# Performance work log

Hardware: AMD Instinct MI355X
Metric: run time of the kernel (lower is better)

## Reference

```python
import jax, jax.numpy as jnp
import numpy as np

N_NODES = 20000   # atoms
N_EDGES = 300000  # directed edges within cutoff
N_TRIP = 500000   # triplets (k->j->i)
H = 128           # hidden_channels
NR = 6            # num_radial
NS = 7            # num_spherical
NB = 8            # num_bilinear
OUT = 128         # out_channels
NLAY = 3          # num_layers in OutputBlock
NOB = 2           # num_blocks + 1 output blocks


def _silu(v):
    return v * jax.nn.sigmoid(v)  # swish


def setup_inputs() -> dict:
    key = jax.random.key(0)
    ks = jax.random.split(key, 20)
    s = lambda fan: np.float32(1.0 / np.sqrt(fan))
    inp = {}
    inp["x"] = jax.random.normal(ks[0], (N_EDGES, H), jnp.float32)
    inp["rbf"] = jax.random.uniform(ks[1], (N_EDGES, NR), jnp.float32)
    inp["sbf"] = jax.random.uniform(ks[2], (N_TRIP, NS * NR), jnp.float32)
    inp["i"] = jax.random.randint(ks[3], (N_EDGES,), 0, N_NODES)
    inp["idx_kj"] = jax.random.randint(ks[4], (N_TRIP,), 0, N_EDGES)
    inp["idx_ji"] = jax.random.randint(ks[5], (N_TRIP,), 0, N_EDGES)
    # Interaction params (weights stored [in, out] so y = x @ W)
    inp["W_rbf"] = jax.random.normal(ks[6], (NR, H), jnp.float32) * s(NR)
    inp["W_sbf"] = jax.random.normal(ks[7], (NS * NR, NB), jnp.float32) * s(NS * NR)
    inp["W_kj"] = jax.random.normal(ks[8], (H, H), jnp.float32) * s(H)
    inp["b_kj"] = jnp.zeros((H,), jnp.float32)
    inp["W_ji"] = jax.random.normal(ks[9], (H, H), jnp.float32) * s(H)
    inp["b_ji"] = jnp.zeros((H,), jnp.float32)
    inp["W_bil"] = jax.random.normal(ks[10], (H, NB, H), jnp.float32) * np.float32(2.0 / H)
    inp["W_lin"] = jax.random.normal(ks[11], (H, H), jnp.float32) * s(H)
    inp["b_lin"] = jnp.zeros((H,), jnp.float32)
    # OutputBlock params, stacked over the NOB blocks
    inp["out_lin_rbf"] = jax.random.normal(ks[12], (NOB, NR, H), jnp.float32) * s(NR)
    inp["out_lins_W"] = jax.random.normal(ks[13], (NOB, NLAY, H, H), jnp.float32) * s(H)
    inp["out_lins_b"] = jnp.zeros((NOB, NLAY, H), jnp.float32)
    inp["out_lin"] = jax.random.normal(ks[14], (NOB, H, OUT), jnp.float32) * s(H)
    return inp


def _output_block(xe, rbf, i, lin_rbf, lins_W, lins_b, lin_out):
    # OutputBlock.forward: gate edge features by rbf projection, scatter to nodes
    g = (rbf @ lin_rbf) * xe              # [E, H]
    g = jax.ops.segment_sum(g, i, num_segments=N_NODES)  # [N, H]
    for li in range(NLAY):
        g = _silu(g @ lins_W[li] + lins_b[li])
    return g @ lin_out                    # [N, OUT]


def _interaction(x, rbf, sbf, idx_kj, idx_ji,
                 W_rbf, W_sbf, W_kj, b_kj, W_ji, b_ji, W_bil, W_lin, b_lin):
    r = rbf @ W_rbf                       # [E, H]
    sproj = sbf @ W_sbf                   # [T, NB]
    x_ji = _silu(x @ W_ji + b_ji)         # [E, H]
    x_kj = _silu(x @ W_kj + b_kj) * r     # [E, H]
    xg = x_kj[idx_kj]                     # [T, H] triplet gather
    # einsum('wj,wl,ijl->wi', sproj, xg, W_bil) without the [T, H, NB] blowup:
    # loop over the small fixed bilinear dim NB, accumulating [T, H]
    t = jnp.zeros((xg.shape[0], H), xg.dtype)
    for jb in range(NB):
        t = t + sproj[:, jb:jb + 1] * (xg @ W_bil[:, jb, :].T)
    agg = jax.ops.segment_sum(t, idx_ji, num_segments=N_EDGES)  # scatter to edges
    return _silu((x_ji + agg) @ W_lin + b_lin)


def reference(x, rbf, sbf, i, idx_kj, idx_ji,
              W_rbf, W_sbf, W_kj, b_kj, W_ji, b_ji, W_bil, W_lin, b_lin,
              out_lin_rbf, out_lins_W, out_lins_b, out_lin):
    P = _output_block(x, rbf, i, out_lin_rbf[0], out_lins_W[0], out_lins_b[0], out_lin[0])
    x2 = _interaction(x, rbf, sbf, idx_kj, idx_ji,
                      W_rbf, W_sbf, W_kj, b_kj, W_ji, b_ji, W_bil, W_lin, b_lin)
    P = P + _output_block(x2, rbf, i, out_lin_rbf[1], out_lins_W[1], out_lins_b[1], out_lin[1])
    return P.sum(axis=0)  # batch=None path: global readout [OUT]
```

## Files before the change

### kernel.cpp

```cpp
#include <hip/hip_runtime.h>
#include <hip/hip_fp16.h>

#define NN 20000
#define NE 300000
#define NT 500000
#define HD 128
#define NRR 6
#define NSNRD 42
#define NBB 8

using f16x8 = __attribute__((ext_vector_type(8))) _Float16;
using f32x4 = __attribute__((ext_vector_type(4))) float;

__device__ __forceinline__ float silu_f(float v){ return v / (1.f + __expf(-v)); }

__device__ __forceinline__ void pk_add(__half2* p, float lo, float hi){
  __half2 h = __floats2half2_rn(lo, hi);
  unsigned int b = *reinterpret_cast<unsigned int*>(&h);
  asm volatile("global_atomic_pk_add_f16 %0, %1, off" :: "v"(p), "v"(b) : "memory");
}

__device__ __forceinline__ void gload16(const void* g, char* lds_dst){
  __builtin_amdgcn_global_load_lds(
    (const __attribute__((address_space(1))) void*)g,
    (__attribute__((address_space(3))) void*)lds_dst, 16, 0, 0);
}

__global__ void k_x16(const float* __restrict__ x, __half* __restrict__ xh){
  long i = ((long)blockIdx.x*256 + threadIdx.x)*8;
  if(i < (long)NE*HD){
    float4 a = *(const float4*)(x+i), b = *(const float4*)(x+i+4);
    __half h8[8];
    h8[0]=__float2half(a.x); h8[1]=__float2half(a.y);
    h8[2]=__float2half(a.z); h8[3]=__float2half(a.w);
    h8[4]=__float2half(b.x); h8[5]=__float2half(b.y);
    h8[6]=__float2half(b.z); h8[7]=__float2half(b.w);
    *(float4*)(xh+i) = *(float4*)h8;
  }
}

__global__ void k_wb2(const float* __restrict__ Wb, __half* __restrict__ WB2){
  int idx = blockIdx.x*256 + threadIdx.x;
  int l = idx & 127, i = (idx>>7) & 127, jb = idx>>14;
  WB2[jb*16384 + i*128 + l] = __float2half(Wb[i*1024 + jb*128 + l]);
}

__global__ void k_wT(const float* __restrict__ Wkj, const float* __restrict__ Wji,
                     const float* __restrict__ Wlin, __half* __restrict__ WkjT,
                     __half* __restrict__ WjiT, __half* __restrict__ WlinT){
  int idx = blockIdx.x*256 + threadIdx.x;
  int which = idx>>14, rem = idx & 16383;
  int i = rem>>7, k = rem & 127;
  const float* src = which==0 ? Wkj : (which==1 ? Wji : Wlin);
  __half* dst = which==0 ? WkjT : (which==1 ? WjiT : WlinT);
  dst[rem] = __float2half(src[k*HD + i]);
}

__global__ void k_wT6(const float* __restrict__ olW, __half* __restrict__ dst){
  int idx = blockIdx.x*256 + threadIdx.x;
  int lw = idx>>14, rem = idx & 16383;
  int i = rem>>7, k = rem & 127;
  dst[lw*16384 + rem] = __float2half(olW[lw*16384 + k*HD + i]);
}

#define EROWS 128
#define PRE_A 0
#define PRE_B 32768
#define PRE_RBF 65536
#define PRE_WR 68608
#define PRE_LS 71680
#define PRE_NID 74752
#define SH_PRE 75264
__global__ __launch_bounds__(512,4)
void k_edge_pre(const __half* __restrict__ xh, const float* __restrict__ rbf,
                const int* __restrict__ nid, const __half* __restrict__ WkjT,
                const float* __restrict__ bkj, const float* __restrict__ Wrbf,
                const float* __restrict__ lrbf0, __half* __restrict__ xkj,
                __half* __restrict__ g0){
  extern __shared__ char sm[];
  int tid = threadIdx.x;
  long e0 = (long)blockIdx.x * EROWS;
  for(int c=tid;c<2048;c+=512){
    int i=c>>4, cc=c&15;
    float4 v = *(const float4*)(WkjT + i*128 + cc*8);
    *(float4*)(sm + PRE_B + ((i*256+cc*16)^((i&7)<<4))) = v;
  }
  for(int c=tid;c<2048;c+=512){
    int r=c>>4, cc=c&15; long e=e0+r;
    float4 v = (e<NE) ? *(const float4*)(xh + e*HD + cc*8)
                      : (float4){0.f,0.f,0.f,0.f};
    *(float4*)(sm + PRE_A + ((r*256+cc*16)^((r&7)<<4))) = v;
  }
  float* rbft=(float*)(sm+PRE_RBF);
  for(int q=tid;q<EROWS*NRR;q+=512){ long e=e0+q/NRR; rbft[q]=(e<NE)? rbf[e*NRR + q%NRR] : 0.f; }
  float* wrbf=(float*)(sm+PRE_WR);
  for(int q=tid;q<NRR*HD;q+=512) wrbf[q]=Wrbf[q];
  float* ls0=(float*)(sm+PRE_LS);
  for(int q=tid;q<NRR*HD;q+=512) ls0[q]=lrbf0[q];
  int* nids=(int*)(sm+PRE_NID);
  if (tid < EROWS){ long e=e0+tid; nids[tid]=(e<NE)? nid[e] : 0; }
  __syncthreads();
  int lane=tid&63, wid=tid>>6, wr=wid>>1, wc=wid&1;
  f16x8 af[2][4];
  #pragma unroll
  for(int rt=0;rt<2;rt++){
    int r = wr*32 + rt*16 + (lane&15);
    #pragma unroll
    for(int ks=0;ks<4;ks++)
      af[rt][ks] = *(const f16x8*)(sm + PRE_A + ((r*256 + (ks*4+(lane>>4))*16)^((r&7)<<4)));
  }
  f32x4 acc[2][4];
  #pragma unroll
  for(int rt=0;rt<2;rt++){
    #pragma unroll
    for(int ct=0;ct<4;ct++) acc[rt][ct]=(f32x4){0.f,0.f,0.f,0.f};
  }
  #pragma unroll
  for(int ct=0;ct<4;ct++){
    int i = wc*64 + ct*16 + (lane&15);
    #pragma unroll
    for(int ks=0;ks<4;ks++){
      f16x8 b = *(const f16x8*)(sm + PRE_B + ((i*256 + (ks*4+(lane>>4))*16)^((i&7)<<4)));
      acc[0][ct] = __builtin_amdgcn_mfma_f32_16x16x32_f16(af[0][ks], b, acc[0][ct], 0,0,0);
      acc[1][ct] = __builtin_amdgcn_mfma_f32_16x16x32_f16(af[1][ks], b, acc[1][ct], 0,0,0);
    }
  }
  #pragma unroll
  for(int rt=0;rt<2;rt++){
    #pragma unroll
    for(int j=0;j<4;j++){
      int rloc = wr*32 + rt*16 + (lane>>4)*4 + j;
      long e = e0 + rloc;
      bool ok = (e<NE);
      int nb = nids[rloc];
      #pragma unroll
      for(int ct=0;ct<4;ct++){
        int h = wc*64 + ct*16 + (lane&15);
        float v = silu_f(acc[rt][ct][j] + bkj[h]);
        float r2=0.f, gate=0.f;
        #pragma unroll
        for(int q=0;q<NRR;q++){
          float rb = rbft[rloc*NRR+q];
          r2   += rb*wrbf[q*HD+h];
          gate += rb*ls0[q*HD+h];
        }
        float xval = __half2float(*(const __half*)(sm + PRE_A +
                       ((rloc*256 + (h>>3)*16)^((rloc&7)<<4)) + (h&7)*2));
        float w1 = v*r2;
        float w2 = gate*xval;
        float p1 = __shfl_xor(w1, 1, 64);
        float p2 = __shfl_xor(w2, 1, 64);
        if(ok && !(lane&1)){
          *(__half2*)(xkj + e*HD + h) = __floats2half2_rn(w1, p1);
          pk_add((__half2*)(g0 + (long)nb*HD + h), w2, p2);
        }
      }
    }
  }
}

#define TROWS 128
#define OFF_BUF 0
#define OFF_SP 49152
#define OFF_KJ 53248
#define OFF_JI 53760
#define OFF_WSB 54272
#define SH_TRIP 55616
__global__ __launch_bounds__(512,4)
void k_triplet_mfma(const __half* __restrict__ xkj, const float* __restrict__ sbf,
                    const float* __restrict__ Wsbf,
                    const int* __restrict__ ikj, const int* __restrict__ iji,
                    const __half* __restrict__ WB2, __half* __restrict__ agg){
  extern __shared__ char sm[];
  int tid = threadIdx.x;
  long t0 = (long)blockIdx.x * TROWS;
  int* kjs = (int*)(sm + OFF_KJ);
  int* jis = (int*)(sm + OFF_JI);
  if (tid < TROWS){
    int ok = (t0 + tid) < NT;
    kjs[tid] = ok ? ikj[t0+tid] : 0;
    jis[tid] = ok ? iji[t0+tid] : -1;
  }
  float* sbuf = (float*)(sm + OFF_BUF);
  for(int q=tid;q<TROWS*NSNRD;q+=512){
    long t = t0 + q/NSNRD;
    sbuf[q] = (t<NT) ? sbf[t*NSNRD + q%NSNRD] : 0.f;
  }
  float* wsb = (float*)(sm + OFF_WSB);
  for(int q=tid;q<NSNRD*NBB;q+=512) wsb[q]=Wsbf[q];
  __syncthreads();
  float* spl = (float*)(sm + OFF_SP);
  {
    int r = tid>>2, j0 = (tid&3)*2;
    float a0=0.f,a1=0.f;
    for(int q=0;q<NSNRD;q++){
      float v = sbuf[r*NSNRD+q];
      a0 += v*wsb[q*NBB+j0];
      a1 += v*wsb[q*NBB+j0+1];
    }
    spl[r*NBB+j0]=a0; spl[r*NBB+j0+1]=a1;
  }
  __syncthreads();
  for(int c=tid;c<TROWS*16;c+=512){
    int w = c>>4, cc = c&15;
    float4 v = *(const float4*)(xkj + (long)kjs[w]*HD + cc*8);
    *(float4*)(sm + OFF_BUF + ((w*256 + cc*16)^((w&7)<<4))) = v;
  }
  __syncthreads();
  int lane = tid & 63;
  int wid = tid>>6, wr = wid>>1, wc = wid&1;
  f16x8 au[2][4];
  #pragma unroll
  for(int rt=0;rt<2;rt++){
    int w = wr*32 + rt*16 + (lane&15);
    #pragma unroll
    for(int ks=0;ks<4;ks++)
      au[rt][ks] = *(const f16x8*)(sm + OFF_BUF + ((w*256 + ks*64 + (lane>>4)*16)^((w&7)<<4)));
  }
  __syncthreads();
  #pragma unroll
  for(int u=0;u<2;u++){
    int c = u*512 + tid;
    int i = c>>3, lc = (c&7) ^ (i&7);
    gload16(WB2 + i*128 + lc*8,
            sm + OFF_BUF + u*8192 + (tid>>6)*1024);
  }
  #pragma unroll
  for(int u=0;u<2;u++){
    int c = u*512 + tid;
    int i = c>>3, lc = (c&7) ^ (i&7);
    gload16(WB2 + i*128 + 64 + lc*8,
            sm + OFF_BUF + 16384 + u*8192 + (tid>>6)*1024);
  }
  f32x4 acc[2][4];
  #pragma unroll
  for(int rt=0;rt<2;rt++){
    #pragma unroll
    for(int ct=0;ct<4;ct++) acc[rt][ct] = (f32x4){0.f,0.f,0.f,0.f};
  }
  float sr[2];
  #pragma unroll
  for(int p=0;p<16;p++){
    int jb = p>>1, h = p&1;
    if(h==0){
      #pragma unroll
      for(int rt=0;rt<2;rt++) sr[rt] = spl[(wr*32 + rt*16 + (lane&15))*NBB + jb];
    }
    if(p<15) asm volatile("s_waitcnt vmcnt(2)" ::: "memory");
    else     asm volatile("s_waitcnt vmcnt(0)" ::: "memory");
    __builtin_amdgcn_s_barrier();
    asm volatile("" ::: "memory");
    if(p+2 < 16){
      int np = p+2, njb = np>>1, nh = np&1;
      #pragma unroll
      for(int u=0;u<2;u++){
        int c = u*512 + tid;
        int i = c>>3, lc = (c&7) ^ (i&7);
        gload16(WB2 + njb*16384 + i*128 + nh*64 + lc*8,
                sm + OFF_BUF + ((p+2)%3)*16384 + u*8192 + (tid>>6)*1024);
      }
    }
    const char* bbase = sm + OFF_BUF + (p%3)*16384;
    #pragma unroll
    for(int ksl=0;ksl<2;ksl++){
      int ks = h*2 + ksl;
      f16x8 as2[2];
      #pragma unroll
      for(int rt=0;rt<2;rt++){
        _Float16 s = (_Float16)sr[rt];
        #pragma unroll
        for(int j=0;j<8;j++) as2[rt][j] = au[rt][ks][j]*s;
      }
      #pragma unroll
      for(int ct=0;ct<4;ct++){
        int it = wc*64 + ct*16 + (lane&15);
        int chunk = (ksl*4 + (lane>>4)) ^ (it&7);
        f16x8 b = *(const f16x8*)(bbase + it*128 + chunk*16);
        #pragma unroll
        for(int rt=0;rt<2;rt++)
          acc[rt][ct] = __builtin_amdgcn_mfma_f32_16x16x32_f16(as2[rt], b, acc[rt][ct], 0,0,0);
      }
    }
  }
  #pragma unroll
  for(int rt=0;rt<2;rt++){
    #pragma unroll
    for(int r=0;r<4;r++){
      int w = wr*32 + rt*16 + (lane>>4)*4 + r;
      int ji = jis[w];
      #pragma unroll
      for(int ct=0;ct<4;ct++){
        float v = acc[rt][ct][r];
        float p = __shfl_xor(v, 1, 64);
        if (ji >= 0 && !(lane&1))
          pk_add((__half2*)(agg + (long)ji*HD + wc*64 + ct*16 + (lane&15)), v, p);
      }
    }
  }
}

#define PO_A 0
#define PO_B 32768
#define PO_RBF 65536
#define PO_LS 68608
#define PO_NID 71680
#define SH_POST 72192
__global__ __launch_bounds__(512,4)
void k_edge_post(const __half* __restrict__ xh, const float* __restrict__ rbf,
                 const __half* __restrict__ aggh, const int* __restrict__ nid,
                 const __half* __restrict__ WjiT, const float* __restrict__ bji,
                 const __half* __restrict__ WlinT, const float* __restrict__ blin,
                 const float* __restrict__ lrbf1, __half* __restrict__ g1){
  extern __shared__ char sm[];
  int tid = threadIdx.x;
  long e0 = (long)blockIdx.x * EROWS;
  for(int c=tid;c<2048;c+=512){
    int i=c>>4, cc=c&15;
    float4 v = *(const float4*)(WjiT + i*128 + cc*8);
    *(float4*)(sm + PO_B + ((i*256+cc*16)^((i&7)<<4))) = v;
  }
  for(int c=tid;c<2048;c+=512){
    int r=c>>4, cc=c&15; long e=e0+r;
    float4 v = (e<NE) ? *(const float4*)(xh + e*HD + cc*8)
                      : (float4){0.f,0.f,0.f,0.f};
    *(float4*)(sm + PO_A + ((r*256+cc*16)^((r&7)<<4))) = v;
  }
  float* rbft=(float*)(sm+PO_RBF);
  for(int q=tid;q<EROWS*NRR;q+=512){ long e=e0+q/NRR; rbft[q]=(e<NE)? rbf[e*NRR + q%NRR] : 0.f; }
  float* ls1=(float*)(sm+PO_LS);
  for(int q=tid;q<NRR*HD;q+=512) ls1[q]=lrbf1[q];
  int* nids=(int*)(sm+PO_NID);
  if (tid < EROWS){ long e=e0+tid; nids[tid]=(e<NE)? nid[e] : 0; }
  __syncthreads();
  int lane=tid&63, wid=tid>>6, wr=wid>>1, wc=wid&1;
  f16x8 af[2][4];
  #pragma unroll
  for(int rt=0;rt<2;rt++){
    int r = wr*32 + rt*16 + (lane&15);
    #pragma unroll
    for(int ks=0;ks<4;ks++)
      af[rt][ks] = *(const f16x8*)(sm + PO_A + ((r*256 + (ks*4+(lane>>4))*16)^((r&7)<<4)));
  }
  f32x4 acc[2][4];
  #pragma unroll
  for(int rt=0;rt<2;rt++){
    #pragma unroll
    for(int ct=0;ct<4;ct++) acc[rt][ct]=(f32x4){0.f,0.f,0.f,0.f};
  }
  #pragma unroll
  for(int ct=0;ct<4;ct++){
    int i = wc*64 + ct*16 + (lane&15);
    #pragma unroll
    for(int ks=0;ks<4;ks++){
      f16x8 b = *(const f16x8*)(sm + PO_B + ((i*256 + (ks*4+(lane>>4))*16)^((i&7)<<4)));
      acc[0][ct] = __builtin_amdgcn_mfma_f32_16x16x32_f16(af[0][ks], b, acc[0][ct], 0,0,0);
      acc[1][ct] = __builtin_amdgcn_mfma_f32_16x16x32_f16(af[1][ks], b, acc[1][ct], 0,0,0);
    }
  }
  __syncthreads();
  #pragma unroll
  for(int rt=0;rt<2;rt++){
    #pragma unroll
    for(int j=0;j<4;j++){
      int rloc = wr*32 + rt*16 + (lane>>4)*4 + j;
      long e = e0 + rloc;
      #pragma unroll
      for(int ct=0;ct<4;ct++){
        int h = wc*64 + ct*16 + (lane&15);
        float v = silu_f(acc[rt][ct][j] + bji[h]);
        v += (e<NE) ? __half2float(aggh[e*HD + h]) : 0.f;
        int byo = ((rloc*256 + (h>>3)*16)^((rloc&7)<<4)) + (h&7)*2;
        *(__half*)(sm + PO_A + byo) = __float2half(v);
      }
    }
  }
  for(int c=tid;c<2048;c+=512){
    int i=c>>4, cc=c&15;
    float4 v = *(const float4*)(WlinT + i*128 + cc*8);
    *(float4*)(sm + PO_B + ((i*256+cc*16)^((i&7)<<4))) = v;
  }
  __syncthreads();
  f16x8 af2[2][4];
  #pragma unroll
  for(int rt=0;rt<2;rt++){
    int r = wr*32 + rt*16 + (lane&15);
    #pragma unroll
    for(int ks=0;ks<4;ks++)
      af2[rt][ks] = *(const f16x8*)(sm + PO_A + ((r*256 + (ks*4+(lane>>4))*16)^((r&7)<<4)));
  }
  f32x4 acc2[2][4];
  #pragma unroll
  for(int rt=0;rt<2;rt++){
    #pragma unroll
    for(int ct=0;ct<4;ct++) acc2[rt][ct]=(f32x4){0.f,0.f,0.f,0.f};
  }
  #pragma unroll
  for(int ct=0;ct<4;ct++){
    int i = wc*64 + ct*16 + (lane&15);
    #pragma unroll
    for(int ks=0;ks<4;ks++){
      f16x8 b = *(const f16x8*)(sm + PO_B + ((i*256 + (ks*4+(lane>>4))*16)^((i&7)<<4)));
      acc2[0][ct] = __builtin_amdgcn_mfma_f32_16x16x32_f16(af2[0][ks], b, acc2[0][ct], 0,0,0);
      acc2[1][ct] = __builtin_amdgcn_mfma_f32_16x16x32_f16(af2[1][ks], b, acc2[1][ct], 0,0,0);
    }
  }
  #pragma unroll
  for(int rt=0;rt<2;rt++){
    #pragma unroll
    for(int j=0;j<4;j++){
      int rloc = wr*32 + rt*16 + (lane>>4)*4 + j;
      long e = e0 + rloc;
      bool ok = (e<NE);
      int nb = nids[rloc];
      #pragma unroll
      for(int ct=0;ct<4;ct++){
        int h = wc*64 + ct*16 + (lane&15);
        float x2 = silu_f(acc2[rt][ct][j] + blin[h]);
        float gate = 0.f;
        #pragma unroll
        for(int q=0;q<NRR;q++) gate += rbft[rloc*NRR+q]*ls1[q*HD+h];
        float w = gate*x2;
        float p = __shfl_xor(w, 1, 64);
        if(ok && !(lane&1))
          pk_add((__half2*)(g1 + (long)nb*HD + h), w, p);
      }
    }
  }
}

#define SH_MLPM 65536
template<bool LAST>
__global__ __launch_bounds__(512,4)
void k_mlp_mfma(const __half* __restrict__ gin, const __half* __restrict__ WT,
                const float* __restrict__ b, __half* __restrict__ gout,
                float* __restrict__ s){
  extern __shared__ char sm[];
  int tid = threadIdx.x;
  long r0 = (long)blockIdx.x * EROWS;
  for(int c=tid;c<2048;c+=512){
    int i=c>>4, cc=c&15;
    float4 v = *(const float4*)(WT + i*128 + cc*8);
    *(float4*)(sm + 32768 + ((i*256+cc*16)^((i&7)<<4))) = v;
  }
  for(int c=tid;c<2048;c+=512){
    int r=c>>4, cc=c&15; long rr=r0+r;
    float4 v;
    if(rr<NN) v = *(const float4*)(gin + rr*HD + cc*8);
    else      v = (float4){0.f,0.f,0.f,0.f};
    *(float4*)(sm + ((r*256+cc*16)^((r&7)<<4))) = v;
  }
  __syncthreads();
  int lane=tid&63, wid=tid>>6, wr=wid>>1, wc=wid&1;
  f16x8 af[2][4];
  #pragma unroll
  for(int rt=0;rt<2;rt++){
    int r = wr*32 + rt*16 + (lane&15);
    #pragma unroll
    for(int ks=0;ks<4;ks++)
      af[rt][ks] = *(const f16x8*)(sm + ((r*256 + (ks*4+(lane>>4))*16)^((r&7)<<4)));
  }
  f32x4 acc[2][4];
  #pragma unroll
  for(int rt=0;rt<2;rt++){
    #pragma unroll
    for(int ct=0;ct<4;ct++) acc[rt][ct]=(f32x4){0.f,0.f,0.f,0.f};
  }
  #pragma unroll
  for(int ct=0;ct<4;ct++){
    int i = wc*64 + ct*16 + (lane&15);
    #pragma unroll
    for(int ks=0;ks<4;ks++){
      f16x8 bfr = *(const f16x8*)(sm + 32768 + ((i*256 + (ks*4+(lane>>4))*16)^((i&7)<<4)));
      acc[0][ct] = __builtin_amdgcn_mfma_f32_16x16x32_f16(af[0][ks], bfr, acc[0][ct], 0,0,0);
      acc[1][ct] = __builtin_amdgcn_mfma_f32_16x16x32_f16(af[1][ks], bfr, acc[1][ct], 0,0,0);
    }
  }
  if(LAST){
    float vsum[4];
    #pragma unroll
    for(int ct=0;ct<4;ct++) vsum[ct]=0.f;
    #pragma unroll
    for(int rt=0;rt<2;rt++){
      #pragma unroll
      for(int j=0;j<4;j++){
        int rloc = wr*32 + rt*16 + (lane>>4)*4 + j;
        long rr = r0 + rloc;
        #pragma unroll
        for(int ct=0;ct<4;ct++){
          int h = wc*64 + ct*16 + (lane&15);
          float v = (rr<NN) ? silu_f(acc[rt][ct][j] + b[h]) : 0.f;
          vsum[ct] += v;
        }
      }
    }
    #pragma unroll
    for(int ct=0;ct<4;ct++){
      vsum[ct] += __shfl_xor(vsum[ct], 16, 64);
      vsum[ct] += __shfl_xor(vsum[ct], 32, 64);
    }
    if((lane>>4)==0){
      #pragma unroll
      for(int ct=0;ct<4;ct++)
        atomicAdd(&s[wc*64 + ct*16 + (lane&15)], vsum[ct]);
    }
  } else {
    #pragma unroll
    for(int rt=0;rt<2;rt++){
      #pragma unroll
      for(int j=0;j<4;j++){
        int rloc = wr*32 + rt*16 + (lane>>4)*4 + j;
        long rr = r0 + rloc;
        bool ok = (rr<NN);
        #pragma unroll
        for(int ct=0;ct<4;ct++){
          int h = wc*64 + ct*16 + (lane&15);
          float v = silu_f(acc[rt][ct][j] + b[h]);
          float p = __shfl_xor(v, 1, 64);
          if(ok && !(lane&1))
            *(__half2*)(gout + rr*HD + h) = __floats2half2_rn(v, p);
        }
      }
    }
  }
}

__global__ void k_readout(const float* __restrict__ s0, const float* __restrict__ s1,
                          const float* __restrict__ OL, float* __restrict__ out){
  int o = threadIdx.x;
  float acc=0.f;
  for(int h=0;h<HD;h++) acc += s0[h]*OL[h*HD+o] + s1[h]*OL[HD*HD + h*HD+o];
  out[o] = acc;
}

extern "C" void kernel_launch(void* const* d_in, const int* in_sizes, int n_in,
                              void* d_out, int out_size, void* d_ws, size_t ws_size,
                              hipStream_t stream) {
  const float* x     = (const float*)d_in[0];
  const float* rbf   = (const float*)d_in[1];
  const float* sbf   = (const float*)d_in[2];
  const int*   nid   = (const int*)d_in[3];
  const int*   ikj   = (const int*)d_in[4];
  const int*   iji   = (const int*)d_in[5];
  const float* W_rbf = (const float*)d_in[6];
  const float* W_sbf = (const float*)d_in[7];
  const float* W_kj  = (const float*)d_in[8];
  const float* b_kj  = (const float*)d_in[9];
  const float* W_ji  = (const float*)d_in[10];
  const float* b_ji  = (const float*)d_in[11];
  const float* W_bil = (const float*)d_in[12];
  const float* W_lin = (const float*)d_in[13];
  const float* b_lin = (const float*)d_in[14];
  const float* olrbf = (const float*)d_in[15];
  const float* olW   = (const float*)d_in[16];
  const float* olb   = (const float*)d_in[17];
  const float* olin  = (const float*)d_in[18];
  float* out = (float*)d_out;

  size_t off = 0;
  auto alloc = [&](size_t bytes)->size_t{ size_t r = off; off = (off + bytes + 255) & ~(size_t)255; return r; };
  size_t o_xkj  = alloc((size_t)NE*HD*2);
  size_t o_xh   = alloc((size_t)NE*HD*2);
  size_t o_agg  = alloc((size_t)NE*HD*2);
  size_t o_wb2  = alloc((size_t)NBB*HD*HD*2);
  size_t o_wkjT = alloc((size_t)HD*HD*2);
  size_t o_wjiT = alloc((size_t)HD*HD*2);
  size_t o_wlinT= alloc((size_t)HD*HD*2);
  size_t o_wo6  = alloc((size_t)6*HD*HD*2);
  size_t o_g0   = alloc((size_t)NN*HD*2);
  size_t o_g1   = alloc((size_t)NN*HD*2);
  size_t o_gt   = alloc((size_t)NN*HD*2);
  size_t o_s0   = alloc(512);
  size_t o_s1   = alloc(512);
  if (off > ws_size) return;
  char* ws = (char*)d_ws;
  __half* xkj  = (__half*)(ws + o_xkj);
  __half* xh   = (__half*)(ws + o_xh);
  __half* agg  = (__half*)(ws + o_agg);
  __half* wb2  = (__half*)(ws + o_wb2);
  __half* wkjT = (__half*)(ws + o_wkjT);
  __half* wjiT = (__half*)(ws + o_wjiT);
  __half* wlinT= (__half*)(ws + o_wlinT);
  __half* wo6  = (__half*)(ws + o_wo6);
  __half* g0   = (__half*)(ws + o_g0);
  __half* g1   = (__half*)(ws + o_g1);
  __half* gt   = (__half*)(ws + o_gt);
  float* s0    = (float*)(ws + o_s0);
  float* s1    = (float*)(ws + o_s1);

  const void* fmlp0; { auto* p = k_mlp_mfma<false>; fmlp0 = (const void*)p; }
  const void* fmlp1; { auto* p = k_mlp_mfma<true>;  fmlp1 = (const void*)p; }
  hipFuncSetAttribute((const void*)k_edge_pre,     hipFuncAttributeMaxDynamicSharedMemorySize, SH_PRE);
  hipFuncSetAttribute((const void*)k_edge_post,    hipFuncAttributeMaxDynamicSharedMemorySize, SH_POST);
  hipFuncSetAttribute((const void*)k_triplet_mfma, hipFuncAttributeMaxDynamicSharedMemorySize, SH_TRIP);
  hipFuncSetAttribute(fmlp0, hipFuncAttributeMaxDynamicSharedMemorySize, SH_MLPM);
  hipFuncSetAttribute(fmlp1, hipFuncAttributeMaxDynamicSharedMemorySize, SH_MLPM);

  hipMemsetAsync(agg, 0, (size_t)NE*HD*2, stream);
  hipMemsetAsync(g0,  0, (size_t)NN*HD*2, stream);
  hipMemsetAsync(g1,  0, (size_t)NN*HD*2, stream);
  hipMemsetAsync(s0,  0, 512, stream);
  hipMemsetAsync(s1,  0, 512, stream);

  k_x16<<<(int)(((long)NE*HD/8 + 255)/256),256,0,stream>>>(x, xh);
  k_wb2<<<512,256,0,stream>>>(W_bil, wb2);
  k_wT<<<192,256,0,stream>>>(W_kj, W_ji, W_lin, wkjT, wjiT, wlinT);
  k_wT6<<<384,256,0,stream>>>(olW, wo6);

  k_edge_pre<<<(NE+EROWS-1)/EROWS,512,SH_PRE,stream>>>(xh, rbf, nid, wkjT, b_kj, W_rbf,
                                                       olrbf, xkj, g0);
  k_triplet_mfma<<<(NT+TROWS-1)/TROWS,512,SH_TRIP,stream>>>(xkj, sbf, W_sbf, ikj, iji, wb2, agg);
  k_edge_post<<<(NE+EROWS-1)/EROWS,512,SH_POST,stream>>>(xh, rbf, agg, nid, wjiT, b_ji,
                                                         wlinT, b_lin, olrbf + NRR*HD, g1);

  int mlpg = (NN+EROWS-1)/EROWS;
  k_mlp_mfma<false><<<mlpg,512,SH_MLPM,stream>>>(g0, wo6 + 0*16384, olb + 0*128, gt, nullptr);
  k_mlp_mfma<false><<<mlpg,512,SH_MLPM,stream>>>(gt, wo6 + 1*16384, olb + 1*128, g0, nullptr);
  k_mlp_mfma<true ><<<mlpg,512,SH_MLPM,stream>>>(g0, wo6 + 2*16384, olb + 2*128, nullptr, s0);

  k_mlp_mfma<false><<<mlpg,512,SH_MLPM,stream>>>(g1, wo6 + 3*16384, olb + 3*128, gt, nullptr);
  k_mlp_mfma<false><<<mlpg,512,SH_MLPM,stream>>>(gt, wo6 + 4*16384, olb + 4*128, g1, nullptr);
  k_mlp_mfma<true ><<<mlpg,512,SH_MLPM,stream>>>(g1, wo6 + 5*16384, olb + 5*128, nullptr, s1);

  k_readout<<<1,128,0,stream>>>(s0, s1, olin, out);
}
```

Before: 789.2 us.

## Fuse output MLP chain into one kernel and merge weight prep kernels

Replaces the six per-layer output MLP launches with one kernel. Each block keeps its 128-row tile in LDS across all three layers and handles both output blocks, so the intermediate node features never go to global memory. The three weight-conversion kernels are merged into one launch. The triplet kernel's sbf projection is now stored as fp16 in shared memory, which cuts LDS use and removes a conversion. The cost is extra synchronisation inside the fused MLP and slightly lower precision on the triplet scaling factor.

```diff
diff --git a/kernel.cpp b/kernel.cpp
--- a/kernel.cpp
+++ b/kernel.cpp
@@ -39,28 +39,29 @@
   }
 }
 
-__global__ void k_wb2(const float* __restrict__ Wb, __half* __restrict__ WB2){
-  int idx = blockIdx.x*256 + threadIdx.x;
-  int l = idx & 127, i = (idx>>7) & 127, jb = idx>>14;
-  WB2[jb*16384 + i*128 + l] = __float2half(Wb[i*1024 + jb*128 + l]);
-}
-
-__global__ void k_wT(const float* __restrict__ Wkj, const float* __restrict__ Wji,
-                     const float* __restrict__ Wlin, __half* __restrict__ WkjT,
-                     __half* __restrict__ WjiT, __half* __restrict__ WlinT){
-  int idx = blockIdx.x*256 + threadIdx.x;
-  int which = idx>>14, rem = idx & 16383;
-  int i = rem>>7, k = rem & 127;
-  const float* src = which==0 ? Wkj : (which==1 ? Wji : Wlin);
-  __half* dst = which==0 ? WkjT : (which==1 ? WjiT : WlinT);
-  dst[rem] = __float2half(src[k*HD + i]);
-}
-
-__global__ void k_wT6(const float* __restrict__ olW, __half* __restrict__ dst){
-  int idx = blockIdx.x*256 + threadIdx.x;
-  int lw = idx>>14, rem = idx & 16383;
-  int i = rem>>7, k = rem & 127;
-  dst[lw*16384 + rem] = __float2half(olW[lw*16384 + k*HD + i]);
+__global__ void k_prep(const float* __restrict__ Wb, __half* __restrict__ WB2,
+                       const float* __restrict__ Wkj, const float* __restrict__ Wji,
+                       const float* __restrict__ Wlin, __half* __restrict__ WkjT,
+                       __half* __restrict__ WjiT, __half* __restrict__ WlinT,
+                       const float* __restrict__ olW, __half* __restrict__ wo6){
+  int bid = blockIdx.x, tid = threadIdx.x;
+  if(bid < 512){
+    int idx = bid*256 + tid;
+    int l = idx & 127, i = (idx>>7) & 127, jb = idx>>14;
+    WB2[jb*16384 + i*128 + l] = __float2half(Wb[i*1024 + jb*128 + l]);
+  } else if(bid < 704){
+    int idx = (bid-512)*256 + tid;
+    int which = idx>>14, rem = idx & 16383;
+    int i = rem>>7, k = rem & 127;
+    const float* src = which==0 ? Wkj : (which==1 ? Wji : Wlin);
+    __half* dst = which==0 ? WkjT : (which==1 ? WjiT : WlinT);
+    dst[rem] = __float2half(src[k*HD + i]);
+  } else {
+    int idx = (bid-704)*256 + tid;
+    int lw = idx>>14, rem = idx & 16383;
+    int i = rem>>7, k = rem & 127;
+    wo6[lw*16384 + rem] = __float2half(olW[lw*16384 + k*HD + i]);
+  }
 }
 
 #define EROWS 128
@@ -162,10 +163,10 @@
 #define TROWS 128
 #define OFF_BUF 0
 #define OFF_SP 49152
-#define OFF_KJ 53248
-#define OFF_JI 53760
-#define OFF_WSB 54272
-#define SH_TRIP 55616
+#define OFF_KJ 51200
+#define OFF_JI 51712
+#define OFF_WSB 52224
+#define SH_TRIP 53568
 __global__ __launch_bounds__(512,4)
 void k_triplet_mfma(const __half* __restrict__ xkj, const float* __restrict__ sbf,
                     const float* __restrict__ Wsbf,
@@ -189,7 +190,7 @@
   float* wsb = (float*)(sm + OFF_WSB);
   for(int q=tid;q<NSNRD*NBB;q+=512) wsb[q]=Wsbf[q];
   __syncthreads();
-  float* spl = (float*)(sm + OFF_SP);
+  __half* spl = (__half*)(sm + OFF_SP);
   {
     int r = tid>>2, j0 = (tid&3)*2;
     float a0=0.f,a1=0.f;
@@ -198,7 +199,7 @@
       a0 += v*wsb[q*NBB+j0];
       a1 += v*wsb[q*NBB+j0+1];
     }
-    spl[r*NBB+j0]=a0; spl[r*NBB+j0+1]=a1;
+    spl[r*NBB+j0]=__float2half(a0); spl[r*NBB+j0+1]=__float2half(a1);
   }
   __syncthreads();
   for(int c=tid;c<TROWS*16;c+=512){
@@ -238,13 +239,14 @@
     #pragma unroll
     for(int ct=0;ct<4;ct++) acc[rt][ct] = (f32x4){0.f,0.f,0.f,0.f};
   }
-  float sr[2];
+  _Float16 sr[2];
   #pragma unroll
   for(int p=0;p<16;p++){
     int jb = p>>1, h = p&1;
     if(h==0){
       #pragma unroll
-      for(int rt=0;rt<2;rt++) sr[rt] = spl[(wr*32 + rt*16 + (lane&15))*NBB + jb];
+      for(int rt=0;rt<2;rt++)
+        sr[rt] = *(const _Float16*)&spl[(wr*32 + rt*16 + (lane&15))*NBB + jb];
     }
     if(p<15) asm volatile("s_waitcnt vmcnt(2)" ::: "memory");
     else     asm volatile("s_waitcnt vmcnt(0)" ::: "memory");
@@ -267,9 +269,8 @@
       f16x8 as2[2];
       #pragma unroll
       for(int rt=0;rt<2;rt++){
-        _Float16 s = (_Float16)sr[rt];
         #pragma unroll
-        for(int j=0;j<8;j++) as2[rt][j] = au[rt][ks][j]*s;
+        for(int j=0;j<8;j++) as2[rt][j] = au[rt][ks][j]*sr[rt];
       }
       #pragma unroll
       for(int ct=0;ct<4;ct++){
@@ -428,20 +429,18 @@
   }
 }
 
-#define SH_MLPM 65536
-template<bool LAST>
+#define SH_MLPC 65536
 __global__ __launch_bounds__(512,4)
-void k_mlp_mfma(const __half* __restrict__ gin, const __half* __restrict__ WT,
-                const float* __restrict__ b, __half* __restrict__ gout,
-                float* __restrict__ s){
+void k_mlp_chain(const __half* __restrict__ g0, const __half* __restrict__ g1,
+                 const __half* __restrict__ wo6, const float* __restrict__ olb,
+                 float* __restrict__ s0, float* __restrict__ s1){
   extern __shared__ char sm[];
   int tid = threadIdx.x;
-  long r0 = (long)blockIdx.x * EROWS;
-  for(int c=tid;c<2048;c+=512){
-    int i=c>>4, cc=c&15;
-    float4 v = *(const float4*)(WT + i*128 + cc*8);
-    *(float4*)(sm + 32768 + ((i*256+cc*16)^((i&7)<<4))) = v;
-  }
+  int nblk = (NN+EROWS-1)/EROWS;
+  int which = blockIdx.x / nblk;
+  long r0 = (long)(blockIdx.x % nblk) * EROWS;
+  const __half* gin = which ? g1 : g0;
+  float* s = which ? s1 : s0;
   for(int c=tid;c<2048;c+=512){
     int r=c>>4, cc=c&15; long rr=r0+r;
     float4 v;
@@ -449,76 +448,83 @@
     else      v = (float4){0.f,0.f,0.f,0.f};
     *(float4*)(sm + ((r*256+cc*16)^((r&7)<<4))) = v;
   }
-  __syncthreads();
   int lane=tid&63, wid=tid>>6, wr=wid>>1, wc=wid&1;
-  f16x8 af[2][4];
-  #pragma unroll
-  for(int rt=0;rt<2;rt++){
-    int r = wr*32 + rt*16 + (lane&15);
-    #pragma unroll
-    for(int ks=0;ks<4;ks++)
-      af[rt][ks] = *(const f16x8*)(sm + ((r*256 + (ks*4+(lane>>4))*16)^((r&7)<<4)));
-  }
-  f32x4 acc[2][4];
-  #pragma unroll
-  for(int rt=0;rt<2;rt++){
-    #pragma unroll
-    for(int ct=0;ct<4;ct++) acc[rt][ct]=(f32x4){0.f,0.f,0.f,0.f};
-  }
-  #pragma unroll
-  for(int ct=0;ct<4;ct++){
-    int i = wc*64 + ct*16 + (lane&15);
-    #pragma unroll
-    for(int ks=0;ks<4;ks++){
-      f16x8 bfr = *(const f16x8*)(sm + 32768 + ((i*256 + (ks*4+(lane>>4))*16)^((i&7)<<4)));
-      acc[0][ct] = __builtin_amdgcn_mfma_f32_16x16x32_f16(af[0][ks], bfr, acc[0][ct], 0,0,0);
-      acc[1][ct] = __builtin_amdgcn_mfma_f32_16x16x32_f16(af[1][ks], bfr, acc[1][ct], 0,0,0);
-    }
-  }
-  if(LAST){
-    float vsum[4];
-    #pragma unroll
-    for(int ct=0;ct<4;ct++) vsum[ct]=0.f;
+  for(int L=0; L<3; ++L){
+    const __half* WT = wo6 + (which*3+L)*16384;
+    const float* b   = olb + (which*3+L)*128;
+    for(int c=tid;c<2048;c+=512){
+      int i=c>>4, cc=c&15;
+      float4 v = *(const float4*)(WT + i*128 + cc*8);
+      *(float4*)(sm + 32768 + ((i*256+cc*16)^((i&7)<<4))) = v;
+    }
+    __syncthreads();
+    f16x8 af[2][4];
     #pragma unroll
     for(int rt=0;rt<2;rt++){
-      #pragma unroll
-      for(int j=0;j<4;j++){
-        int rloc = wr*32 + rt*16 + (lane>>4)*4 + j;
-        long rr = r0 + rloc;
+      int r = wr*32 + rt*16 + (lane&15);
+      #pragma unroll
+      for(int ks=0;ks<4;ks++)
+        af[rt][ks] = *(const f16x8*)(sm + ((r*256 + (ks*4+(lane>>4))*16)^((r&7)<<4)));
+    }
+    f32x4 acc[2][4];
+    #pragma unroll
+    for(int rt=0;rt<2;rt++){
+      #pragma unroll
+      for(int ct=0;ct<4;ct++) acc[rt][ct]=(f32x4){0.f,0.f,0.f,0.f};
+    }
+    #pragma unroll
+    for(int ct=0;ct<4;ct++){
+      int i = wc*64 + ct*16 + (lane&15);
+      #pragma unroll
+      for(int ks=0;ks<4;ks++){
+        f16x8 bfr = *(const f16x8*)(sm + 32768 + ((i*256 + (ks*4+(lane>>4))*16)^((i&7)<<4)));
+        acc[0][ct] = __builtin_amdgcn_mfma_f32_16x16x32_f16(af[0][ks], bfr, acc[0][ct], 0,0,0);
+        acc[1][ct] = __builtin_amdgcn_mfma_f32_16x16x32_f16(af[1][ks], bfr, acc[1][ct], 0,0,0);
+      }
+    }
+    __syncthreads();
+    if(L < 2){
+      #pragma unroll
+      for(int rt=0;rt<2;rt++){
         #pragma unroll
-        for(int ct=0;ct<4;ct++){
-          int h = wc*64 + ct*16 + (lane&15);
-          float v = (rr<NN) ? silu_f(acc[rt][ct][j] + b[h]) : 0.f;
-          vsum[ct] += v;
+        for(int j=0;j<4;j++){
+          int rloc = wr*32 + rt*16 + (lane>>4)*4 + j;
+          #pragma unroll
+          for(int ct=0;ct<4;ct++){
+            int h = wc*64 + ct*16 + (lane&15);
+            float v = silu_f(acc[rt][ct][j] + b[h]);
+            int byo = ((rloc*256 + (h>>3)*16)^((rloc&7)<<4)) + (h&7)*2;
+            *(__half*)(sm + byo) = __float2half(v);
+          }
         }
       }
-    }
-    #pragma unroll
-    for(int ct=0;ct<4;ct++){
-      vsum[ct] += __shfl_xor(vsum[ct], 16, 64);
-      vsum[ct] += __shfl_xor(vsum[ct], 32, 64);
-    }
-    if((lane>>4)==0){
-      #pragma unroll
-      for(int ct=0;ct<4;ct++)
-        atomicAdd(&s[wc*64 + ct*16 + (lane&15)], vsum[ct]);
-    }
-  } else {
-    #pragma unroll
-    for(int rt=0;rt<2;rt++){
-      #pragma unroll
-      for(int j=0;j<4;j++){
-        int rloc = wr*32 + rt*16 + (lane>>4)*4 + j;
-        long rr = r0 + rloc;
-        bool ok = (rr<NN);
+    } else {
+      float vsum[4];
+      #pragma unroll
+      for(int ct=0;ct<4;ct++) vsum[ct]=0.f;
+      #pragma unroll
+      for(int rt=0;rt<2;rt++){
         #pragma unroll
-        for(int ct=0;ct<4;ct++){
-          int h = wc*64 + ct*16 + (lane&15);
-          float v = silu_f(acc[rt][ct][j] + b[h]);
-          float p = __shfl_xor(v, 1, 64);
-          if(ok && !(lane&1))
-            *(__half2*)(gout + rr*HD + h) = __floats2half2_rn(v, p);
+        for(int j=0;j<4;j++){
+          int rloc = wr*32 + rt*16 + (lane>>4)*4 + j;
+          long rr = r0 + rloc;
+          #pragma unroll
+          for(int ct=0;ct<4;ct++){
+            int h = wc*64 + ct*16 + (lane&15);
+            float v = (rr<NN) ? silu_f(acc[rt][ct][j] + b[h]) : 0.f;
+            vsum[ct] += v;
+          }
         }
+      }
+      #pragma unroll
+      for(int ct=0;ct<4;ct++){
+        vsum[ct] += __shfl_xor(vsum[ct], 16, 64);
+        vsum[ct] += __shfl_xor(vsum[ct], 32, 64);
+      }
+      if((lane>>4)==0){
+        #pragma unroll
+        for(int ct=0;ct<4;ct++)
+          atomicAdd(&s[wc*64 + ct*16 + (lane&15)], vsum[ct]);
       }
     }
   }
@@ -568,7 +574,6 @@
   size_t o_wo6  = alloc((size_t)6*HD*HD*2);
   size_t o_g0   = alloc((size_t)NN*HD*2);
   size_t o_g1   = alloc((size_t)NN*HD*2);
-  size_t o_gt   = alloc((size_t)NN*HD*2);
   size_t o_s0   = alloc(512);
   size_t o_s1   = alloc(512);
   if (off > ws_size) return;
@@ -583,17 +588,13 @@
   __half* wo6  = (__half*)(ws + o_wo6);
   __half* g0   = (__half*)(ws + o_g0);
   __half* g1   = (__half*)(ws + o_g1);
-  __half* gt   = (__half*)(ws + o_gt);
   float* s0    = (float*)(ws + o_s0);
   float* s1    = (float*)(ws + o_s1);
 
-  const void* fmlp0; { auto* p = k_mlp_mfma<false>; fmlp0 = (const void*)p; }
-  const void* fmlp1; { auto* p = k_mlp_mfma<true>;  fmlp1 = (const void*)p; }
   hipFuncSetAttribute((const void*)k_edge_pre,     hipFuncAttributeMaxDynamicSharedMemorySize, SH_PRE);
   hipFuncSetAttribute((const void*)k_edge_post,    hipFuncAttributeMaxDynamicSharedMemorySize, SH_POST);
   hipFuncSetAttribute((const void*)k_triplet_mfma, hipFuncAttributeMaxDynamicSharedMemorySize, SH_TRIP);
-  hipFuncSetAttribute(fmlp0, hipFuncAttributeMaxDynamicSharedMemorySize, SH_MLPM);
-  hipFuncSetAttribute(fmlp1, hipFuncAttributeMaxDynamicSharedMemorySize, SH_MLPM);
+  hipFuncSetAttribute((const void*)k_mlp_chain,    hipFuncAttributeMaxDynamicSharedMemorySize, SH_MLPC);
 
   hipMemsetAsync(agg, 0, (size_t)NE*HD*2, stream);
   hipMemsetAsync(g0,  0, (size_t)NN*HD*2, stream);
@@ -602,9 +603,7 @@
   hipMemsetAsync(s1,  0, 512, stream);
 
   k_x16<<<(int)(((long)NE*HD/8 + 255)/256),256,0,stream>>>(x, xh);
-  k_wb2<<<512,256,0,stream>>>(W_bil, wb2);
-  k_wT<<<192,256,0,stream>>>(W_kj, W_ji, W_lin, wkjT, wjiT, wlinT);
-  k_wT6<<<384,256,0,stream>>>(olW, wo6);
+  k_prep<<<1088,256,0,stream>>>(W_bil, wb2, W_kj, W_ji, W_lin, wkjT, wjiT, wlinT, olW, wo6);
 
   k_edge_pre<<<(NE+EROWS-1)/EROWS,512,SH_PRE,stream>>>(xh, rbf, nid, wkjT, b_kj, W_rbf,
                                                        olrbf, xkj, g0);
@@ -613,13 +612,7 @@
                                                          wlinT, b_lin, olrbf + NRR*HD, g1);
 
   int mlpg = (NN+EROWS-1)/EROWS;
-  k_mlp_mfma<false><<<mlpg,512,SH_MLPM,stream>>>(g0, wo6 + 0*16384, olb + 0*128, gt, nullptr);
-  k_mlp_mfma<false><<<mlpg,512,SH_MLPM,stream>>>(gt, wo6 + 1*16384, olb + 1*128, g0, nullptr);
-  k_mlp_mfma<true ><<<mlpg,512,SH_MLPM,stream>>>(g0, wo6 + 2*16384, olb + 2*128, nullptr, s0);
-
-  k_mlp_mfma<false><<<mlpg,512,SH_MLPM,stream>>>(g1, wo6 + 3*16384, olb + 3*128, gt, nullptr);
-  k_mlp_mfma<false><<<mlpg,512,SH_MLPM,stream>>>(gt, wo6 + 4*16384, olb + 4*128, g1, nullptr);
-  k_mlp_mfma<true ><<<mlpg,512,SH_MLPM,stream>>>(g1, wo6 + 5*16384, olb + 5*128, nullptr, s1);
+  k_mlp_chain<<<2*mlpg,512,SH_MLPC,stream>>>(g0, g1, wo6, olb, s0, s1);
 
   k_readout<<<1,128,0,stream>>>(s0, s1, olin, out);
 }
```

New measurement: 736.7 us. -6.7%, faster.
